# Optimization experiments

Hardware: AMD Instinct MI355X
Metric: run time of the kernel (lower is better)

Reference implementation:

```python
import jax, jax.numpy as jnp
import numpy as np

B, L, C = 8, 999, 768
C2 = C // 2           # 384 per branch
H, HD = 8, C2 // 8    # heads, head_dim=48
K, G = 3, 2           # dynamic conv kernel size, num_groups
DC_IN = C2 // 4       # DynamicConv1d proj inner (reduction_ratio default 4) = 96
PJ_IN = max(16, C // 8)  # mixer proj inner_dim = 96
SCALE = HD ** -0.5
EPS = 1e-5


def _gelu(x):
    return jax.nn.gelu(x, approximate=False)


def _c1x1(x, w, b):
    # pointwise conv1d: x (B,Cin,L), w (Cout,Cin), b (Cout,)
    return jnp.einsum('bcl,oc->bol', x, w) + b[None, :, None]


def _dw3(x, w, b):
    # depthwise conv1d k=3 pad=1: x (B,Ch,L), w (Ch,3), b (Ch,) or None
    Lx = x.shape[-1]
    xp = jnp.pad(x, ((0, 0), (0, 0), (1, 1)))
    y = (xp[:, :, 0:Lx] * w[:, 0][None, :, None]
         + xp[:, :, 1:Lx + 1] * w[:, 1][None, :, None]
         + xp[:, :, 2:Lx + 2] * w[:, 2][None, :, None])
    if b is not None:
        y = y + b[None, :, None]
    return y


def _bn(x, g, b):
    # BatchNorm1d, training-mode batch stats over (B, L): x (B,Ch,L)
    m = x.mean(axis=(0, 2), keepdims=True)
    v = ((x - m) ** 2).mean(axis=(0, 2), keepdims=True)
    return (x - m) * jax.lax.rsqrt(v + EPS) * g[None, :, None] + b[None, :, None]


def setup_inputs() -> dict:
    key = jax.random.key(0)
    ks = jax.random.split(key, 30)
    s = 0.02
    d = {
        'x': jax.random.normal(ks[0], (B, L, C), jnp.float32),
        # DynamicConv1d (dim=384, K=3, G=2, inner=96)
        'dc_weight': jax.random.normal(ks[1], (G, C2, K), jnp.float32) * s,
        'dc_bias':   jax.random.normal(ks[2], (G, C2), jnp.float32) * s,
        'dc_p1w':    jax.random.normal(ks[3], (DC_IN, C2), jnp.float32) * s,
        'dc_p1b':    jax.random.normal(ks[4], (DC_IN,), jnp.float32) * s,
        'dc_p2w':    jax.random.normal(ks[5], (C2 * G, DC_IN), jnp.float32) * s,
        'dc_p2b':    jax.random.normal(ks[6], (C2 * G,), jnp.float32) * s,
        # Attention (dim=384, heads=8, sr_ratio=1 -> sr=Identity)
        'at_qw':  jax.random.normal(ks[7], (C2, C2), jnp.float32) * s,
        'at_qb':  jax.random.normal(ks[8], (C2,), jnp.float32) * s,
        'at_kvw': jax.random.normal(ks[9], (2 * C2, C2), jnp.float32) * s,
        'at_kvb': jax.random.normal(ks[10], (2 * C2,), jnp.float32) * s,
        'at_lcw': jax.random.normal(ks[11], (C2, K), jnp.float32) * s,
        'at_lcb': jax.random.normal(ks[12], (C2,), jnp.float32) * s,
        # mixer proj
        'pj_dww':  jax.random.normal(ks[13], (C, K), jnp.float32) * s,
        'pj_dwb':  jax.random.normal(ks[14], (C,), jnp.float32) * s,
        'pj_bn1g': jnp.ones((C,), jnp.float32),
        'pj_bn1b': jnp.zeros((C,), jnp.float32),
        'pj_c1w':  jax.random.normal(ks[15], (PJ_IN, C), jnp.float32) * s,
        'pj_c1b':  jax.random.normal(ks[16], (PJ_IN,), jnp.float32) * s,
        'pj_bn2g': jnp.ones((PJ_IN,), jnp.float32),
        'pj_bn2b': jnp.zeros((PJ_IN,), jnp.float32),
        'pj_c2w':  jax.random.normal(ks[17], (C, PJ_IN), jnp.float32) * s,
        'pj_c2b':  jax.random.normal(ks[18], (C,), jnp.float32) * s,
        'pj_bn3g': jnp.ones((C,), jnp.float32),
        'pj_bn3b': jnp.zeros((C,), jnp.float32),
    }
    return d


def _dynamic_conv(x, dc_weight, dc_bias, p1w, p1b, p2w, p2b):
    # x: (B, L, C2)
    xt = jnp.transpose(x, (0, 2, 1))                 # (B,C2,L)
    # AdaptiveAvgPool1d(K) with L divisible by K -> exact non-overlapping mean
    pooled = xt.reshape(B, C2, K, L // K).mean(-1)   # (B,C2,K)
    sc = _c1x1(_gelu(_c1x1(pooled, p1w, p1b)), p2w, p2b)  # (B, G*C2, K)
    sc = jax.nn.softmax(sc.reshape(B, G, C2, K), axis=1)
    w = (sc * dc_weight[None]).sum(axis=1)           # (B,C2,K) per-sample kernels
    xm = xt.mean(axis=2, keepdims=True)              # (B,C2,1)
    sb = _c1x1(_gelu(_c1x1(xm, p1w, p1b)), p2w, p2b) # (B, G*C2, 1)
    sb = jax.nn.softmax(sb.reshape(B, G, C2), axis=1)
    bias = (sb * dc_bias[None]).sum(axis=1)          # (B,C2)
    # depthwise per-(b,c) conv, k=3, pad=1
    xp = jnp.pad(xt, ((0, 0), (0, 0), (1, 1)))
    y = (xp[:, :, 0:L] * w[:, :, 0:1]
         + xp[:, :, 1:L + 1] * w[:, :, 1:2]
         + xp[:, :, 2:L + 2] * w[:, :, 2:3]) + bias[:, :, None]
    return jnp.transpose(y, (0, 2, 1))               # (B,L,C2)


def _attention(x, qw, qb, kvw, kvb, lcw, lcb):
    # x: (B, L, C2)
    xt = jnp.transpose(x, (0, 2, 1))                 # (B,C2,L)
    q = _c1x1(xt, qw, qb).reshape(B, H, HD, L)
    q = jnp.transpose(q, (0, 1, 3, 2))               # (B,H,L,HD)
    kv_in = _dw3(xt, lcw, lcb) + xt                  # local_conv(kv)+kv (sr=Identity)
    kv = _c1x1(kv_in, kvw, kvb)                      # (B,2*C2,L)
    k = kv[:, :C2].reshape(B, H, HD, L)              # (B,H,HD,L)
    v = jnp.transpose(kv[:, C2:].reshape(B, H, HD, L), (0, 1, 3, 2))  # (B,H,L,HD)
    attn = jnp.einsum('bhld,bhdm->bhlm', q, k) * SCALE
    attn = jax.nn.softmax(attn, axis=-1)
    out = jnp.einsum('bhlm,bhmd->bhld', attn, v)     # (B,H,L,HD)
    # faithful to torch: transpose(-1,-2) then reshape(B, L, C2)
    out = jnp.transpose(out, (0, 1, 3, 2)).reshape(B, L, C2)
    return out


def reference(x, dc_weight, dc_bias, dc_p1w, dc_p1b, dc_p2w, dc_p2b,
              at_qw, at_qb, at_kvw, at_kvb, at_lcw, at_lcb,
              pj_dww, pj_dwb, pj_bn1g, pj_bn1b, pj_c1w, pj_c1b,
              pj_bn2g, pj_bn2b, pj_c2w, pj_c2b, pj_bn3g, pj_bn3b):
    x1 = x[:, :, :C2]
    x2 = x[:, :, C2:]
    x1 = _dynamic_conv(x1, dc_weight, dc_bias, dc_p1w, dc_p1b, dc_p2w, dc_p2b)
    x2 = _attention(x2, at_qw, at_qb, at_kvw, at_kvb, at_lcw, at_lcb)
    xc = jnp.concatenate([x1, x2], axis=2)           # (B,L,C)
    xt = jnp.transpose(xc, (0, 2, 1))                # (B,C,L)
    h = _bn(_gelu(_dw3(xt, pj_dww, pj_dwb)), pj_bn1g, pj_bn1b)
    h = _bn(_gelu(_c1x1(h, pj_c1w, pj_c1b)), pj_bn2g, pj_bn2b)
    h = _bn(_c1x1(h, pj_c2w, pj_c2b), pj_bn3g, pj_bn3b)
    out = h + xt
    return jnp.transpose(out, (0, 2, 1))             # (B,L,C)
```

## Files before the change

### kernel.cpp

```cpp
#include <hip/hip_runtime.h>
#include <cstddef>

constexpr int B = 8, L = 999, C = 768, C2 = 384, H = 8, HD = 48;
constexpr float ATT_SCALE = 0.14433756729740644f;
constexpr float LOG2E = 1.4426950408889634f;
constexpr float BN_EPS = 1e-5f;
constexpr float INV_N = 1.0f / (8.0f * 999.0f);

constexpr size_t SZ_XT   = (size_t)B * C * L;
constexpr size_t SZ_HALF = (size_t)B * C2 * L;
constexpr size_t OFF_XT  = 0;
constexpr size_t OFF_XT2 = SZ_XT;
constexpr size_t OFF_KV  = 2 * SZ_XT;
constexpr size_t OFF_AX  = 3 * SZ_XT;
constexpr size_t OFF_Q   = 3 * SZ_XT + SZ_HALF;
constexpr size_t OFF_SM  = 3 * SZ_XT + SZ_HALF + SZ_HALF / 2;

constexpr size_t SM_POOLED = 0;
constexpr size_t SM_XM     = 9216;
constexpr size_t SM_H1     = 12288;
constexpr size_t SM_WDYN   = 15360;
constexpr size_t SM_BDYN   = 24576;
constexpr size_t SM_SUM1   = 27648;
constexpr size_t SM_SQ1    = 28416;
constexpr size_t SM_S1     = 29184;
constexpr size_t SM_M1     = 29952;
constexpr size_t SM_CB1    = 30720;
constexpr size_t SM_SUM2   = 30816;
constexpr size_t SM_SQ2    = 30912;
constexpr size_t SM_S2     = 31008;
constexpr size_t SM_M2     = 31104;
constexpr size_t SM_CB2    = 31200;
constexpr size_t SM_SUM3   = 31968;
constexpr size_t SM_SQ3    = 32736;
constexpr size_t SM_S3     = 33504;
constexpr size_t SM_D3     = 34272;
constexpr size_t SM_END    = 35040;
constexpr size_t SM_WQ  = SM_END;
constexpr size_t SM_WKV = SM_WQ + 73728;
constexpr size_t SM_WC1 = SM_WKV + 147456;
constexpr size_t SM_WC2 = SM_WC1 + 36864;

typedef __attribute__((ext_vector_type(8))) short bf16x8;
typedef __attribute__((ext_vector_type(4))) float floatx4;

__device__ __forceinline__ float gelu_f(float x) {
  return 0.5f * x * (1.0f + erff(x * 0.70710678118654752f));
}

__device__ __forceinline__ float wave_sum(float v) {
  #pragma unroll
  for (int off = 32; off > 0; off >>= 1) v += __shfl_down(v, off, 64);
  return v;
}

__device__ __forceinline__ short f2bf(float f) {
  union { float f; unsigned u; } x; x.f = f;
  unsigned r = x.u + 0x7FFFu + ((x.u >> 16) & 1u);
  return (short)(r >> 16);
}

__device__ __forceinline__ bf16x8 pack8(const float* p) {
  union { unsigned u[4]; bf16x8 v; } r;
  asm("v_cvt_pk_bf16_f32 %0, %1, %2" : "=v"(r.u[0]) : "v"(p[0]), "v"(p[1]));
  asm("v_cvt_pk_bf16_f32 %0, %1, %2" : "=v"(r.u[1]) : "v"(p[2]), "v"(p[3]));
  asm("v_cvt_pk_bf16_f32 %0, %1, %2" : "=v"(r.u[2]) : "v"(p[4]), "v"(p[5]));
  asm("v_cvt_pk_bf16_f32 %0, %1, %2" : "=v"(r.u[3]) : "v"(p[6]), "v"(p[7]));
  return r.v;
}

__device__ __forceinline__ float exp2_hw(float x) {
  float r;
  asm("v_exp_f32 %0, %1" : "=v"(r) : "v"(x));
  return r;
}

__global__ void k_prep(const float* __restrict__ qw, short* __restrict__ wq,
                       const float* __restrict__ kvw, short* __restrict__ wkv,
                       const float* __restrict__ c1w, short* __restrict__ wc1,
                       const float* __restrict__ c2w, short* __restrict__ wc2,
                       const float* __restrict__ c1b, const float* __restrict__ bn1b,
                       const float* __restrict__ c2b, const float* __restrict__ bn2b,
                       float* __restrict__ cb1, float* __restrict__ cb2) {
  int bid = blockIdx.x;
  if (bid < 288) {
    const float* src; short* dst; int base;
    if (bid < 72)       { src = qw;  dst = wq;  base = bid; }
    else if (bid < 216) { src = kvw; dst = wkv; base = bid - 72; }
    else if (bid < 252) { src = c1w; dst = wc1; base = bid - 216; }
    else                { src = c2w; dst = wc2; base = bid - 252; }
    int i = (base * 256 + threadIdx.x) * 8;
    float4 a = *reinterpret_cast<const float4*>(&src[i]);
    float4 b = *reinterpret_cast<const float4*>(&src[i + 4]);
    short tmp[8] = {f2bf(a.x), f2bf(a.y), f2bf(a.z), f2bf(a.w),
                    f2bf(b.x), f2bf(b.y), f2bf(b.z), f2bf(b.w)};
    *(bf16x8*)&dst[i] = *(bf16x8*)tmp;
  } else if (bid == 288) {
    int o = threadIdx.x;
    if (o < 96) {
      float a = c1b[o];
      const float* wr = c1w + (size_t)o * C;
      for (int c = 0; c < C; c++) a += bn1b[c] * wr[c];
      cb1[o] = a;
    }
  } else {
    for (int o = threadIdx.x; o < C; o += 256) {
      float a = c2b[o];
      const float* wr = c2w + (size_t)o * 96;
      for (int i = 0; i < 96; i++) a += bn2b[i] * wr[i];
      cb2[o] = a;
    }
  }
}

__global__ __launch_bounds__(384) void k_kvin(const float* __restrict__ x,
                                              const float* __restrict__ lcw,
                                              const float* __restrict__ lcb,
                                              short* __restrict__ x2bf,
                                              short* __restrict__ kvinbf) {
  int b = blockIdx.y, l0 = blockIdx.x * 8, c = threadIdx.x;
  float w0 = lcw[c * 3], w1 = lcw[c * 3 + 1] + 1.0f, w2 = lcw[c * 3 + 2], bb = lcb[c];
  const float* xb = x + (size_t)b * L * C + C2 + c;
  float prev = (l0 > 0) ? xb[(size_t)(l0 - 1) * C] : 0.f;
  float cur  = (l0 < L) ? xb[(size_t)l0 * C] : 0.f;
  #pragma unroll
  for (int r = 0; r < 8; r++) {
    int l = l0 + r;
    if (l >= L) break;
    float nxt = (l + 1 < L) ? xb[(size_t)(l + 1) * C] : 0.f;
    x2bf[((size_t)b * L + l) * C2 + c]   = f2bf(cur);
    kvinbf[((size_t)b * L + l) * C2 + c] = f2bf(prev * w0 + cur * w1 + nxt * w2 + bb);
    prev = cur; cur = nxt;
  }
}

__global__ void k_transpose_in(const float* __restrict__ x, float* __restrict__ xt) {
  __shared__ float tile[32][33];
  int b = blockIdx.z;
  int l0 = blockIdx.x * 32, c0 = blockIdx.y * 32;
  int tx = threadIdx.x, ty = threadIdx.y;
  #pragma unroll
  for (int i = 0; i < 4; i++) {
    int l = l0 + ty + i * 8, c = c0 + tx;
    if (l < L) tile[ty + i * 8][tx] = x[((size_t)b * L + l) * C + c];
  }
  __syncthreads();
  #pragma unroll
  for (int i = 0; i < 4; i++) {
    int c = c0 + ty + i * 8, l = l0 + tx;
    if (l < L) xt[((size_t)b * C + c) * L + l] = tile[tx][ty + i * 8];
  }
}

__global__ __launch_bounds__(256) void k_pool(const float* __restrict__ xt,
                                              float* __restrict__ pooled,
                                              float* __restrict__ xm) {
  int c = blockIdx.x, b = blockIdx.y;
  const float* row = xt + ((size_t)b * C + c) * L;
  float s0 = 0.f, s1 = 0.f, s2 = 0.f;
  for (int l = threadIdx.x; l < L; l += 256) {
    float v = row[l];
    int ch = l / 333;
    if (ch == 0) s0 += v; else if (ch == 1) s1 += v; else s2 += v;
  }
  s0 = wave_sum(s0); s1 = wave_sum(s1); s2 = wave_sum(s2);
  __shared__ float r[3][4];
  int lane = threadIdx.x & 63, wid = threadIdx.x >> 6;
  if (lane == 0) { r[0][wid] = s0; r[1][wid] = s1; r[2][wid] = s2; }
  __syncthreads();
  if (threadIdx.x == 0) {
    float t0 = r[0][0] + r[0][1] + r[0][2] + r[0][3];
    float t1 = r[1][0] + r[1][1] + r[1][2] + r[1][3];
    float t2 = r[2][0] + r[2][1] + r[2][2] + r[2][3];
    size_t pb = (size_t)(b * C2 + c) * 3;
    pooled[pb + 0] = t0 / 333.f;
    pooled[pb + 1] = t1 / 333.f;
    pooled[pb + 2] = t2 / 333.f;
    xm[b * C2 + c] = (t0 + t1 + t2) / 999.f;
  }
}

__global__ void k_mlp1(const float* __restrict__ pooled, const float* __restrict__ xm,
                       const float* __restrict__ p1w, const float* __restrict__ p1b,
                       float* __restrict__ h1) {
  int j = blockIdx.x, b = blockIdx.y;
  __shared__ float vin[C2];
  for (int c = threadIdx.x; c < C2; c += 128)
    vin[c] = (j < 3) ? pooled[(size_t)(b * C2 + c) * 3 + j] : xm[b * C2 + c];
  __syncthreads();
  int o = threadIdx.x;
  if (o < 96) {
    float acc = p1b[o];
    const float* wr = p1w + (size_t)o * C2;
    for (int c = 0; c < C2; c++) acc += vin[c] * wr[c];
    h1[(b * 4 + j) * 96 + o] = gelu_f(acc);
  }
}

__global__ void k_mix2(const float* __restrict__ h1,
                       const float* __restrict__ p2w, const float* __restrict__ p2b,
                       const float* __restrict__ dcw, const float* __restrict__ dcb,
                       float* __restrict__ wdyn, float* __restrict__ bdyn) {
  int j = blockIdx.x, b = blockIdx.y;
  __shared__ float hv[96];
  for (int i = threadIdx.x; i < 96; i += 384) hv[i] = h1[(b * 4 + j) * 96 + i];
  __syncthreads();
  int c = threadIdx.x;
  float a0 = p2b[c], a1 = p2b[C2 + c];
  const float* w0r = p2w + (size_t)c * 96;
  const float* w1r = p2w + (size_t)(C2 + c) * 96;
  for (int i = 0; i < 96; i++) { float h = hv[i]; a0 += h * w0r[i]; a1 += h * w1r[i]; }
  float m = fmaxf(a0, a1);
  float e0 = __expf(a0 - m), e1 = __expf(a1 - m);
  float inv = 1.f / (e0 + e1);
  float p0 = e0 * inv, p1 = e1 * inv;
  if (j < 3)
    wdyn[(size_t)(b * C2 + c) * 3 + j] = p0 * dcw[(size_t)c * 3 + j] + p1 * dcw[(size_t)(C2 + c) * 3 + j];
  else
    bdyn[b * C2 + c] = p0 * dcb[c] + p1 * dcb[C2 + c];
}

__global__ __launch_bounds__(256) void k_dwconv(const float* __restrict__ xt,
                                                const float* __restrict__ wdyn,
                                                const float* __restrict__ bdyn,
                                                float* __restrict__ xt2) {
  int c = blockIdx.x, b = blockIdx.y;
  const float* rowA = xt + ((size_t)b * C + c) * L;
  size_t wb = (size_t)(b * C2 + c) * 3;
  float a0 = wdyn[wb], a1 = wdyn[wb + 1], a2 = wdyn[wb + 2], ab = bdyn[b * C2 + c];
  float* oA = xt2 + ((size_t)b * C + c) * L;
  for (int l = threadIdx.x; l < L; l += 256) {
    float xm1 = (l > 0) ? rowA[l - 1] : 0.f;
    float x0 = rowA[l];
    float xp1 = (l < L - 1) ? rowA[l + 1] : 0.f;
    oA[l] = xm1 * a0 + x0 * a1 + xp1 * a2 + ab;
  }
}

template<int LT, bool XBF16>
__global__ __launch_bounds__(256) void k_gemm3(const short* __restrict__ Wbf,
                                               const void* __restrict__ Xv,
                                               void* __restrict__ Yv,
                                               const float* __restrict__ shift,
                                               const float* __restrict__ scale,
                                               const float* __restrict__ bias,
                                               float* __restrict__ sum, float* __restrict__ sq,
                                               int O, int Kd, int Kstride, int XLd,
                                               size_t xbs, size_t ybs,
                                               int flags, float outmul,
                                               int ksplit, size_t slice) {
  __shared__ __align__(16) short Xt[2][LT * 72];
  constexpr int R = LT / 32;
  int b = blockIdx.z;
  int kc = (int)blockIdx.y % ksplit;
  int o0 = ((int)blockIdx.y / ksplit) * 64;
  int l0 = blockIdx.x * LT;
  int kbeg = kc * Kd;
  int t = threadIdx.x, w = t >> 6, lane = t & 63;
  int col = lane & 15, quad = lane >> 4;
  int KT = (Kd + 63) >> 6;

  floatx4 acc[LT / 16];
  #pragma unroll
  for (int i = 0; i < LT / 16; i++) acc[i] = floatx4{0.f, 0.f, 0.f, 0.f};

  int orow = o0 + w * 16 + col;
  bool wok = orow < O;
  const short* Wrow = Wbf + (size_t)orow * Kstride + kbeg;

  const short* Xb16 = (const short*)Xv + (size_t)b * xbs + kbeg;
  const float* Xb32 = (const float*)Xv + (size_t)b * xbs + kbeg;

  bf16x8 xr[R];
  float4 xf[R][2];
  bf16x8 wcur0, wcur1, wnxt0, wnxt1;

  auto xload = [&](int k0) {
    #pragma unroll
    for (int r = 0; r < R; r++) {
      int u = t + r * 256;
      int ll = u >> 3, oct = u & 7;
      int l = l0 + ll, kk = k0 + oct * 8;
      bool ok = (l < L) && (kk < Kd);
      if constexpr (XBF16) {
        xr[r] = ok ? *(const bf16x8*)&Xb16[(size_t)l * XLd + kk]
                   : bf16x8{0, 0, 0, 0, 0, 0, 0, 0};
      } else {
        if (ok) {
          const float* p = &Xb32[(size_t)l * XLd + kk];
          float4 a = *(const float4*)p;
          float4 bq = *(const float4*)(p + 4);
          if (shift) {
            float4 sh0 = *(const float4*)&shift[kbeg + kk];
            float4 sh1 = *(const float4*)&shift[kbeg + kk + 4];
            float4 sc0 = *(const float4*)&scale[kbeg + kk];
            float4 sc1 = *(const float4*)&scale[kbeg + kk + 4];
            a.x = (a.x - sh0.x) * sc0.x;  a.y = (a.y - sh0.y) * sc0.y;
            a.z = (a.z - sh0.z) * sc0.z;  a.w = (a.w - sh0.w) * sc0.w;
            bq.x = (bq.x - sh1.x) * sc1.x; bq.y = (bq.y - sh1.y) * sc1.y;
            bq.z = (bq.z - sh1.z) * sc1.z; bq.w = (bq.w - sh1.w) * sc1.w;
          }
          xf[r][0] = a;
          xf[r][1] = bq;
        } else {
          xf[r][0] = float4{0.f, 0.f, 0.f, 0.f};
          xf[r][1] = float4{0.f, 0.f, 0.f, 0.f};
        }
      }
    }
  };
  auto xwrite = [&](int buf) {
    #pragma unroll
    for (int r = 0; r < R; r++) {
      int u = t + r * 256;
      int ll = u >> 3, oct = u & 7;
      bf16x8 val;
      if constexpr (XBF16) {
        val = xr[r];
      } else {
        union { unsigned u4[4]; bf16x8 v; } pk;
        asm("v_cvt_pk_bf16_f32 %0, %1, %2" : "=v"(pk.u4[0]) : "v"(xf[r][0].x), "v"(xf[r][0].y));
        asm("v_cvt_pk_bf16_f32 %0, %1, %2" : "=v"(pk.u4[1]) : "v"(xf[r][0].z), "v"(xf[r][0].w));
        asm("v_cvt_pk_bf16_f32 %0, %1, %2" : "=v"(pk.u4[2]) : "v"(xf[r][1].x), "v"(xf[r][1].y));
        asm("v_cvt_pk_bf16_f32 %0, %1, %2" : "=v"(pk.u4[3]) : "v"(xf[r][1].z), "v"(xf[r][1].w));
        val = pk.v;
      }
      *(bf16x8*)&Xt[buf][ll * 72 + oct * 8] = val;
    }
  };
  auto wload = [&](int k0, bf16x8& f0, bf16x8& f1) {
    int kk0 = k0 + quad * 8;
    int kk1 = k0 + 32 + quad * 8;
    f0 = (wok && kk0 < Kd) ? *(const bf16x8*)&Wrow[kk0] : bf16x8{0, 0, 0, 0, 0, 0, 0, 0};
    f1 = (wok && kk1 < Kd) ? *(const bf16x8*)&Wrow[kk1] : bf16x8{0, 0, 0, 0, 0, 0, 0, 0};
  };

  xload(0);
  wload(0, wcur0, wcur1);
  xwrite(0);
  __syncthreads();

  for (int it = 0; it < KT; ++it) {
    int curb = it & 1;
    bool more = (it + 1 < KT);
    if (more) { xload((it + 1) * 64); wload((it + 1) * 64, wnxt0, wnxt1); }
    #pragma unroll
    for (int nt = 0; nt < LT / 16; nt++) {
      bf16x8 bx0 = *(bf16x8*)&Xt[curb][(nt * 16 + col) * 72 + quad * 8];
      acc[nt] = __builtin_amdgcn_mfma_f32_16x16x32_bf16(wcur0, bx0, acc[nt], 0, 0, 0);
      bf16x8 bx1 = *(bf16x8*)&Xt[curb][(nt * 16 + col) * 72 + 32 + quad * 8];
      acc[nt] = __builtin_amdgcn_mfma_f32_16x16x32_bf16(wcur1, bx1, acc[nt], 0, 0, 0);
    }
    if (more) xwrite(curb ^ 1);
    __syncthreads();
    wcur0 = wnxt0; wcur1 = wnxt1;
  }

  int o_base = o0 + w * 16 + quad * 4;
  #pragma unroll
  for (int r = 0; r < 4; r++) {
    int o = o_base + r;
    bool ov = o < O;
    float bo = (bias && ov) ? bias[o] : 0.f;
    float ps = 0.f, pq = 0.f;
    #pragma unroll
    for (int nt = 0; nt < LT / 16; nt++) {
      int l = l0 + nt * 16 + col;
      float v = acc[nt][r] + bo;
      if (flags & 1) v = gelu_f(v);
      v *= outmul;
      if (l >= L) v = 0.f;
      if (ov && l < L) {
        if (flags & 2) ((short*)Yv)[(size_t)b * ybs + (size_t)o * L + l] = f2bf(v);
        else           ((float*)Yv)[kc * slice + (size_t)b * ybs + (size_t)o * L + l] = v;
      }
      ps += v; pq += v * v;
    }
    if ((flags & 8) && ov) {
      ps += __shfl_xor(ps, 1); ps += __shfl_xor(ps, 2);
      ps += __shfl_xor(ps, 4); ps += __shfl_xor(ps, 8);
      pq += __shfl_xor(pq, 1); pq += __shfl_xor(pq, 2);
      pq += __shfl_xor(pq, 4); pq += __shfl_xor(pq, 8);
      if (col == 0) { atomicAdd(&sum[o], ps); atomicAdd(&sq[o], pq); }
    }
  }
}

__global__ __launch_bounds__(256) void k_h2fin_t(const float* __restrict__ part,
                                                 const float* __restrict__ cb1,
                                                 float* __restrict__ h2,
                                                 float* __restrict__ sum, float* __restrict__ sq) {
  __shared__ float tile[96][33];
  __shared__ float lsum[96], lsq[96];
  constexpr size_t SL = (size_t)B * 96 * L;
  int b = blockIdx.y, l0 = blockIdx.x * 32;
  int t = threadIdx.x;
  #pragma unroll
  for (int p = 0; p < 12; p++) {
    int u = t + p * 256;
    int o = u >> 5, li = u & 31;
    int l = l0 + li;
    float v = 0.f;
    if (l < L) {
      size_t idx = ((size_t)b * 96 + o) * L + l;
      v = gelu_f(part[idx] + part[SL + idx] + part[2 * SL + idx] + part[3 * SL + idx] + cb1[o]);
    }
    tile[o][li] = v;
    float vs = v, vq = v * v;
    vs += __shfl_xor(vs, 1); vs += __shfl_xor(vs, 2); vs += __shfl_xor(vs, 4);
    vs += __shfl_xor(vs, 8); vs += __shfl_xor(vs, 16);
    vq += __shfl_xor(vq, 1); vq += __shfl_xor(vq, 2); vq += __shfl_xor(vq, 4);
    vq += __shfl_xor(vq, 8); vq += __shfl_xor(vq, 16);
    if ((t & 31) == 0) { lsum[o] = vs; lsq[o] = vq; }
  }
  __syncthreads();
  if (t < 96) { atomicAdd(&sum[t], lsum[t]); atomicAdd(&sq[t], lsq[t]); }
  #pragma unroll
  for (int p = 0; p < 12; p++) {
    int u = t + p * 256;
    int lr = u / 96, o = u % 96;
    int l = l0 + lr;
    if (l < L) h2[((size_t)b * L + l) * 96 + o] = tile[o][lr];
  }
}

__global__ __launch_bounds__(512, 4) void k_attn_mfma(const short* __restrict__ q,
                                                      const short* __restrict__ kv,
                                                      float* __restrict__ out) {
  __shared__ __align__(16) char smem[2 * 8192 + 2 * 6144 + 33280];
  short* Ks0 = (short*)smem;
  short* Ks1 = (short*)(smem + 8192);
  short* Vf0 = (short*)(smem + 16384);
  short* Vf1 = (short*)(smem + 22528);
  float* PF  = (float*)(smem + 28672);
  float* Os  = (float*)smem;

  int lt0 = blockIdx.x * 128;
  int h = blockIdx.y, b = blockIdx.z;
  int t = threadIdx.x;
  int w = t >> 6, lane = t & 63;
  int col = lane & 15, quad = lane >> 4;
  const short* qb = q  + ((size_t)b * C2 + h * HD) * L;
  const short* kb = kv + ((size_t)b * C  + h * HD) * L;
  const short* vb = kv + ((size_t)b * C + C2 + h * HD) * L;

  bf16x8 aq0, aq1;
  {
    int l = lt0 + w * 16 + col;
    bool ok = l < L;
    const short* qp = qb + (size_t)(quad * 8) * L + l;
    short v0[8];
    #pragma unroll
    for (int jj = 0; jj < 8; jj++) v0[jj] = ok ? qp[(size_t)jj * L] : (short)0;
    aq0 = *(bf16x8*)v0;
    if (quad < 2) {
      const short* qp1 = qb + (size_t)(32 + quad * 8) * L + l;
      short v1[8];
      #pragma unroll
      for (int jj = 0; jj < 8; jj++) v1[jj] = ok ? qp1[(size_t)jj * L] : (short)0;
      aq1 = *(bf16x8*)v1;
    } else {
      aq1 = bf16x8{0, 0, 0, 0, 0, 0, 0, 0};
    }
  }

  short kreg[8];
  short vreg[8];

  auto stage_load = [&](int m0) {
    if (t < 384) {
      int m = t & 63, j = t >> 6;
      int gm = m0 + m;
      bool ok = gm < L;
      const short* src = kb + (size_t)(8 * j) * L + gm;
      #pragma unroll
      for (int jj = 0; jj < 8; jj++) kreg[jj] = ok ? src[(size_t)jj * L] : (short)0;
    }
    if (t >= 128) {
      int a = t - 128;
      int d = (a & 7) | ((a >> 6) << 3);
      int o = (a >> 3) & 7;
      int mb = m0 + o * 8;
      const short* src = vb + (size_t)d * L + mb;
      #pragma unroll
      for (int j = 0; j < 8; j++) vreg[j] = (mb + j < L) ? src[j] : (short)0;
    }
  };
  auto stage_write = [&](short* Kd, short* Vd) {
    if (t < 384) {
      int m = t & 63, j = t >> 6;
      int slot = ((m >> 4) * 2 + (j >> 2)) * 64 + (j & 3) * 16 + (m & 15);
      *(bf16x8*)&Kd[slot * 8] = *(bf16x8*)kreg;
    }
    if (t >= 128) {
      int a = t - 128;
      int d = (a & 7) | ((a >> 6) << 3);
      int o = (a >> 3) & 7;
      int lanep = ((o & 3) << 4) | (d & 15);
      *(bf16x8*)&Vd[(((o >> 2) * 3 + (d >> 4)) * 64 + lanep) * 8] = *(bf16x8*)vreg;
    }
  };

  if (t < 256) {
    int i = t & 127;
    int ms = i >> 5, qq = 2 + ((i >> 4) & 1), cc = i & 15;
    int slot = (ms * 2 + 1) * 64 + qq * 16 + cc;
    short* Kd = (t < 128) ? Ks0 : Ks1;
    *(bf16x8*)&Kd[slot * 8] = bf16x8{0, 0, 0, 0, 0, 0, 0, 0};
  }

  stage_load(0);
  stage_write(Ks0, Vf0);

  floatx4 of[3];
  #pragma unroll
  for (int i = 0; i < 3; i++) of[i] = floatx4{0.f, 0.f, 0.f, 0.f};
  float rs[4] = {0.f, 0.f, 0.f, 0.f};
  __syncthreads();

  for (int it = 0; it < 16; ++it) {
    int m0 = it * 64;
    short* Kc = (it & 1) ? Ks1 : Ks0;
    short* Vc = (it & 1) ? Vf1 : Vf0;
    short* Kn = (it & 1) ? Ks0 : Ks1;
    short* Vn = (it & 1) ? Vf0 : Vf1;
    if (it < 15) stage_load(m0 + 64);

    floatx4 sf[4];
    __builtin_amdgcn_s_setprio(1);
    #pragma unroll
    for (int ms = 0; ms < 4; ms++) {
      bf16x8 bk0 = *(bf16x8*)&Kc[((ms * 2 + 0) * 64 + lane) * 8];
      bf16x8 bk1 = *(bf16x8*)&Kc[((ms * 2 + 1) * 64 + lane) * 8];
      floatx4 a4 = floatx4{0.f, 0.f, 0.f, 0.f};
      a4 = __builtin_amdgcn_mfma_f32_16x16x32_bf16(aq0, bk0, a4, 0, 0, 0);
      a4 = __builtin_amdgcn_mfma_f32_16x16x32_bf16(aq1, bk1, a4, 0, 0, 0);
      sf[ms] = a4;
    }
    __builtin_amdgcn_s_setprio(0);

    float* pw = PF + w * 1040 + lane;
    #pragma unroll
    for (int ms = 0; ms < 4; ms++) {
      int m = m0 + ms * 16 + col;
      bool ok = m < L;
      #pragma unroll
      for (int r = 0; r < 4; r++) {
        float e = ok ? exp2_hw(sf[ms][r]) : 0.f;
        rs[r] += e;
        pw[(ms * 4 + r) * 65] = e;
      }
    }

    const float* pr = PF + w * 1040 + (col & 3) * 65 + (col >> 2) * 16 + (quad & 1) * 8;
    __builtin_amdgcn_s_setprio(1);
    #pragma unroll
    for (int mh = 0; mh < 2; mh++) {
      const float* ps = pr + (mh * 2 + (quad >> 1)) * 260;
      float p8[8];
      #pragma unroll
      for (int jj = 0; jj < 8; jj++) p8[jj] = ps[jj];
      bf16x8 ap = pack8(p8);
      #pragma unroll
      for (int ds = 0; ds < 3; ds++) {
        bf16x8 bv = *(bf16x8*)&Vc[((mh * 3 + ds) * 64 + lane) * 8];
        of[ds] = __builtin_amdgcn_mfma_f32_16x16x32_bf16(ap, bv, of[ds], 0, 0, 0);
      }
    }
    __builtin_amdgcn_s_setprio(0);
    if (it < 15) stage_write(Kn, Vn);
    __syncthreads();
  }

  #pragma unroll
  for (int r = 0; r < 4; r++) {
    float v = rs[r];
    v += __shfl_xor(v, 1); v += __shfl_xor(v, 2);
    v += __shfl_xor(v, 4); v += __shfl_xor(v, 8);
    rs[r] = v;
  }
  #pragma unroll
  for (int r = 0; r < 4; r++) {
    float inv = 1.f / rs[r];
    #pragma unroll
    for (int ds = 0; ds < 3; ds++)
      Os[(ds * 16 + col) * 130 + w * 16 + quad * 4 + r] = of[ds][r] * inv;
  }
  __syncthreads();
  for (int i = t; i < 48 * 128; i += 512) {
    int d = i >> 7, ll = i & 127;
    int l = lt0 + ll;
    if (l < L) out[((size_t)b * C2 + h * HD + d) * L + l] = Os[d * 130 + ll];
  }
}

__global__ void k_fill_xt2(const float* __restrict__ ao, float* __restrict__ xt2) {
  __shared__ float tile[32][33];
  int b = blockIdx.z;
  int l0 = blockIdx.x * 32, c0 = blockIdx.y * 32;
  int tx = threadIdx.x, ty = threadIdx.y;
  #pragma unroll
  for (int i = 0; i < 4; i++) {
    int l = l0 + ty + i * 8, c = c0 + tx;
    if (l < L) tile[ty + i * 8][tx] = ao[(size_t)b * ((size_t)L * C2) + (size_t)l * C2 + c];
  }
  __syncthreads();
  #pragma unroll
  for (int i = 0; i < 4; i++) {
    int c = c0 + ty + i * 8, l = l0 + tx;
    if (l < L) xt2[((size_t)b * C + C2 + c) * L + l] = tile[tx][ty + i * 8];
  }
}

__global__ __launch_bounds__(256) void k_dwproj_t(const float* __restrict__ xt2,
                                                  const float* __restrict__ dww,
                                                  const float* __restrict__ dwb,
                                                  float* __restrict__ t1,
                                                  float* __restrict__ sum, float* __restrict__ sq) {
  __shared__ float tile[32][67];
  __shared__ float rs[4][32], rq[4][32];
  int b = blockIdx.z, c0 = blockIdx.y * 32, l0 = blockIdx.x * 64;
  int t = threadIdx.x;
  for (int u = t; u < 32 * 66; u += 256) {
    int cc = u / 66, li = u % 66;
    int l = l0 - 1 + li;
    tile[cc][li] = (l >= 0 && l < L) ? xt2[((size_t)b * C + c0 + cc) * L + l] : 0.f;
  }
  __syncthreads();
  int c = c0 + (t & 31);
  float w0 = dww[c * 3], w1 = dww[c * 3 + 1], w2 = dww[c * 3 + 2], bb = dwb[c];
  int cc = t & 31;
  float s = 0.f, s2 = 0.f;
  #pragma unroll
  for (int p = 0; p < 8; p++) {
    int lr = (t >> 5) + p * 8;
    int l = l0 + lr;
    float v = 0.f;
    if (l < L) {
      v = gelu_f(tile[cc][lr] * w0 + tile[cc][lr + 1] * w1 + tile[cc][lr + 2] * w2 + bb);
      t1[((size_t)b * L + l) * C + c] = v;
    }
    s += v; s2 += v * v;
  }
  s += __shfl_xor(s, 32, 64); s2 += __shfl_xor(s2, 32, 64);
  int wv = t >> 6, ln = t & 63;
  if (ln < 32) { rs[wv][ln] = s; rq[wv][ln] = s2; }
  __syncthreads();
  if (t < 32) {
    float a = rs[0][t] + rs[1][t] + rs[2][t] + rs[3][t];
    float qq = rq[0][t] + rq[1][t] + rq[2][t] + rq[3][t];
    atomicAdd(&sum[c0 + t], a);
    atomicAdd(&sq[c0 + t], qq);
  }
}

__global__ void k_bnfin(const float* __restrict__ sum, const float* __restrict__ sq,
                        const float* __restrict__ g, int n,
                        float* __restrict__ s_, float* __restrict__ m_) {
  int t = threadIdx.x;
  if (t < n) {
    float m = sum[t] * INV_N;
    float v = sq[t] * INV_N - m * m;
    float r = rsqrtf(v + BN_EPS);
    s_[t] = g[t] * r;
    m_[t] = m;
  }
}

__global__ void k_fin3(const float* __restrict__ sum, const float* __restrict__ sq,
                       const float* __restrict__ g, const float* __restrict__ be,
                       float* __restrict__ s3, float* __restrict__ d3) {
  int t = threadIdx.x;
  if (t < C) {
    float m = sum[t] * INV_N;
    float v = sq[t] * INV_N - m * m;
    float r = rsqrtf(v + BN_EPS);
    float sc = g[t] * r;
    s3[t] = sc;
    d3[t] = be[t] - m * sc;
  }
}

__global__ void k_final(const float* __restrict__ y3, const float* __restrict__ xt2,
                        const float* __restrict__ s3, const float* __restrict__ d3,
                        float* __restrict__ out) {
  __shared__ float tile[32][33];
  int b = blockIdx.z;
  int l0 = blockIdx.x * 32, c0 = blockIdx.y * 32;
  int tx = threadIdx.x, ty = threadIdx.y;
  #pragma unroll
  for (int i = 0; i < 4; i++) {
    int c = c0 + ty + i * 8, l = l0 + tx;
    if (l < L) {
      size_t idx = ((size_t)b * C + c) * L + l;
      tile[ty + i * 8][tx] = y3[idx] * s3[c] + d3[c] + xt2[idx];
    }
  }
  __syncthreads();
  #pragma unroll
  for (int i = 0; i < 4; i++) {
    int l = l0 + ty + i * 8, c = c0 + tx;
    if (l < L) out[((size_t)b * L + l) * C + c] = tile[tx][ty + i * 8];
  }
}

extern "C" void kernel_launch(void* const* d_in, const int* in_sizes, int n_in,
                              void* d_out, int out_size, void* d_ws, size_t ws_size,
                              hipStream_t stream) {
  const float* x    = (const float*)d_in[0];
  const float* dcw  = (const float*)d_in[1];
  const float* dcb  = (const float*)d_in[2];
  const float* p1w  = (const float*)d_in[3];
  const float* p1b  = (const float*)d_in[4];
  const float* p2w  = (const float*)d_in[5];
  const float* p2b  = (const float*)d_in[6];
  const float* qw   = (const float*)d_in[7];
  const float* qb   = (const float*)d_in[8];
  const float* kvw  = (const float*)d_in[9];
  const float* kvb  = (const float*)d_in[10];
  const float* lcw  = (const float*)d_in[11];
  const float* lcb  = (const float*)d_in[12];
  const float* dww  = (const float*)d_in[13];
  const float* dwb  = (const float*)d_in[14];
  const float* bn1g = (const float*)d_in[15];
  const float* bn1b = (const float*)d_in[16];
  const float* c1w  = (const float*)d_in[17];
  const float* c1b  = (const float*)d_in[18];
  const float* bn2g = (const float*)d_in[19];
  const float* bn2b = (const float*)d_in[20];
  const float* c2w  = (const float*)d_in[21];
  const float* c2b  = (const float*)d_in[22];
  const float* bn3g = (const float*)d_in[23];
  const float* bn3b = (const float*)d_in[24];
  float* out = (float*)d_out;
  float* ws  = (float*)d_ws;

  float* xt      = ws + OFF_XT;
  float* xt2     = ws + OFF_XT2;
  short* kvbuf   = (short*)(ws + OFF_KV);
  float* y3      = ws + OFF_KV;
  short* x2bf    = (short*)(ws + OFF_AX);
  short* kvinbf  = (short*)(ws + OFF_AX + SZ_HALF / 2);
  float* attnout = ws + OFF_AX;
  float* c1part  = ws + OFF_AX;
  short* qbuf    = (short*)(ws + OFF_Q);
  float* h2      = ws + OFF_Q;
  float* sm      = ws + OFF_SM;

  float* pooled = sm + SM_POOLED;
  float* xm     = sm + SM_XM;
  float* h1     = sm + SM_H1;
  float* wdyn   = sm + SM_WDYN;
  float* bdyn   = sm + SM_BDYN;
  float* sum1 = sm + SM_SUM1; float* sq1 = sm + SM_SQ1;
  float* s1 = sm + SM_S1; float* m1 = sm + SM_M1; float* cb1 = sm + SM_CB1;
  float* sum2 = sm + SM_SUM2; float* sq2 = sm + SM_SQ2;
  float* s2 = sm + SM_S2; float* m2 = sm + SM_M2; float* cb2 = sm + SM_CB2;
  float* sum3 = sm + SM_SUM3; float* sq3 = sm + SM_SQ3;
  float* s3 = sm + SM_S3; float* d3 = sm + SM_D3;
  short* wqbf  = (short*)(sm + SM_WQ);
  short* wkvbf = (short*)(sm + SM_WKV);
  short* wc1bf = (short*)(sm + SM_WC1);
  short* wc2bf = (short*)(sm + SM_WC2);

  hipMemsetAsync((void*)(sm + SM_SUM1), 0, (SM_S3 - SM_SUM1) * sizeof(float), stream);

  k_prep<<<290, 256, 0, stream>>>(qw, wqbf, kvw, wkvbf, c1w, wc1bf, c2w, wc2bf,
                                  c1b, bn1b, c2b, bn2b, cb1, cb2);
  k_kvin<<<dim3(125, B), 384, 0, stream>>>(x, lcw, lcb, x2bf, kvinbf);

  dim3 tb32(32, 8);
  k_transpose_in<<<dim3(32, 12, B), tb32, 0, stream>>>(x, xt);
  k_pool<<<dim3(C2, B), 256, 0, stream>>>(xt, pooled, xm);
  k_mlp1<<<dim3(4, B), 128, 0, stream>>>(pooled, xm, p1w, p1b, h1);
  k_mix2<<<dim3(4, B), 384, 0, stream>>>(h1, p2w, p2b, dcw, dcb, wdyn, bdyn);
  k_dwconv<<<dim3(C2, B), 256, 0, stream>>>(xt, wdyn, bdyn, xt2);
  k_gemm3<64, true><<<dim3(16, 6, B), 256, 0, stream>>>(
      wqbf, (const void*)x2bf, (void*)qbuf, nullptr, nullptr, qb, nullptr, nullptr,
      C2, C2, C2, C2, (size_t)C2 * L, (size_t)C2 * L, 2, ATT_SCALE * LOG2E, 1, 0);
  k_gemm3<128, true><<<dim3(8, 12, B), 256, 0, stream>>>(
      wkvbf, (const void*)kvinbf, (void*)kvbuf, nullptr, nullptr, kvb, nullptr, nullptr,
      C, C2, C2, C2, (size_t)C2 * L, (size_t)C * L, 2, 1.0f, 1, 0);
  k_attn_mfma<<<dim3(8, H, B), 512, 0, stream>>>(qbuf, kvbuf, attnout);
  k_fill_xt2<<<dim3(32, 12, B), tb32, 0, stream>>>(attnout, xt2);
  k_dwproj_t<<<dim3(16, 24, B), 256, 0, stream>>>(xt2, dww, dwb, xt, sum1, sq1);
  k_bnfin<<<1, 768, 0, stream>>>(sum1, sq1, bn1g, C, s1, m1);
  k_gemm3<128, false><<<dim3(8, 8, B), 256, 0, stream>>>(
      wc1bf, (const void*)xt, (void*)c1part, m1, s1, nullptr, nullptr, nullptr,
      96, 192, C, C, (size_t)C * L, (size_t)96 * L, 0, 1.0f, 4, (size_t)B * 96 * L);
  k_h2fin_t<<<dim3(32, B), 256, 0, stream>>>(c1part, cb1, h2, sum2, sq2);
  k_bnfin<<<1, 768, 0, stream>>>(sum2, sq2, bn2g, 96, s2, m2);
  k_gemm3<128, false><<<dim3(8, 12, B), 256, 0, stream>>>(
      wc2bf, (const void*)h2, (void*)y3, m2, s2, cb2, sum3, sq3,
      C, 96, 96, 96, (size_t)96 * L, (size_t)C * L, 8, 1.0f, 1, 0);
  k_fin3<<<1, 768, 0, stream>>>(sum3, sq3, bn3g, bn3b, s3, d3);
  k_final<<<dim3(32, 24, B), tb32, 0, stream>>>(y3, xt2, s3, d3, out);
}
```

Measured before the change: 353.7 us.

## Widen GEMM output tiles and pad KV rows for vectorized V loads

k_gemm3 gains an OT template parameter so each block computes 128 output rows. This reuses each shared-memory X tile across two weight slices and halves the grid for the Q, KV and conv2 GEMMs. The KV projection now writes rows with a padded stride of 1000, so the attention kernel can load V with aligned 16-byte vector loads instead of 8 scalar shorts. The fp32-to-bf16 conversion moves from the LDS write step into the global load step. Costs are more accumulator registers, which can lower occupancy, and fewer blocks in flight.

```diff
diff --git a/kernel.cpp b/kernel.cpp
--- a/kernel.cpp
+++ b/kernel.cpp
@@ -2,6 +2,7 @@
 #include <cstddef>
 
 constexpr int B = 8, L = 999, C = 768, C2 = 384, H = 8, HD = 48;
+constexpr int KVL = 1000;
 constexpr float ATT_SCALE = 0.14433756729740644f;
 constexpr float LOG2E = 1.4426950408889634f;
 constexpr float BN_EPS = 1e-5f;
@@ -237,7 +238,7 @@
   }
 }
 
-template<int LT, bool XBF16>
+template<int LT, int OT, bool XBF16>
 __global__ __launch_bounds__(256) void k_gemm3(const short* __restrict__ Wbf,
                                                const void* __restrict__ Xv,
                                                void* __restrict__ Yv,
@@ -245,35 +246,42 @@
                                                const float* __restrict__ scale,
                                                const float* __restrict__ bias,
                                                float* __restrict__ sum, float* __restrict__ sq,
-                                               int O, int Kd, int Kstride, int XLd,
+                                               int O, int Kd, int Kstride, int XLd, int Ldy,
                                                size_t xbs, size_t ybs,
                                                int flags, float outmul,
                                                int ksplit, size_t slice) {
   __shared__ __align__(16) short Xt[2][LT * 72];
   constexpr int R = LT / 32;
+  constexpr int NS = OT / 64;
   int b = blockIdx.z;
   int kc = (int)blockIdx.y % ksplit;
-  int o0 = ((int)blockIdx.y / ksplit) * 64;
+  int o0 = ((int)blockIdx.y / ksplit) * OT;
   int l0 = blockIdx.x * LT;
   int kbeg = kc * Kd;
   int t = threadIdx.x, w = t >> 6, lane = t & 63;
   int col = lane & 15, quad = lane >> 4;
   int KT = (Kd + 63) >> 6;
 
-  floatx4 acc[LT / 16];
-  #pragma unroll
-  for (int i = 0; i < LT / 16; i++) acc[i] = floatx4{0.f, 0.f, 0.f, 0.f};
-
-  int orow = o0 + w * 16 + col;
-  bool wok = orow < O;
-  const short* Wrow = Wbf + (size_t)orow * Kstride + kbeg;
+  floatx4 acc[NS][LT / 16];
+  #pragma unroll
+  for (int s = 0; s < NS; s++)
+    #pragma unroll
+    for (int i = 0; i < LT / 16; i++) acc[s][i] = floatx4{0.f, 0.f, 0.f, 0.f};
+
+  bool wok[NS];
+  const short* Wrow[NS];
+  #pragma unroll
+  for (int s = 0; s < NS; s++) {
+    int orow = o0 + s * 64 + w * 16 + col;
+    wok[s] = orow < O;
+    Wrow[s] = Wbf + (size_t)orow * Kstride + kbeg;
+  }
 
   const short* Xb16 = (const short*)Xv + (size_t)b * xbs + kbeg;
   const float* Xb32 = (const float*)Xv + (size_t)b * xbs + kbeg;
 
   bf16x8 xr[R];
-  float4 xf[R][2];
-  bf16x8 wcur0, wcur1, wnxt0, wnxt1;
+  bf16x8 wcur[NS][2], wnxt[NS][2];
 
   auto xload = [&](int k0) {
     #pragma unroll
@@ -300,11 +308,14 @@
             bq.x = (bq.x - sh1.x) * sc1.x; bq.y = (bq.y - sh1.y) * sc1.y;
             bq.z = (bq.z - sh1.z) * sc1.z; bq.w = (bq.w - sh1.w) * sc1.w;
           }
-          xf[r][0] = a;
-          xf[r][1] = bq;
+          union { unsigned u4[4]; bf16x8 v; } pk;
+          asm("v_cvt_pk_bf16_f32 %0, %1, %2" : "=v"(pk.u4[0]) : "v"(a.x), "v"(a.y));
+          asm("v_cvt_pk_bf16_f32 %0, %1, %2" : "=v"(pk.u4[1]) : "v"(a.z), "v"(a.w));
+          asm("v_cvt_pk_bf16_f32 %0, %1, %2" : "=v"(pk.u4[2]) : "v"(bq.x), "v"(bq.y));
+          asm("v_cvt_pk_bf16_f32 %0, %1, %2" : "=v"(pk.u4[3]) : "v"(bq.z), "v"(bq.w));
+          xr[r] = pk.v;
         } else {
-          xf[r][0] = float4{0.f, 0.f, 0.f, 0.f};
-          xf[r][1] = float4{0.f, 0.f, 0.f, 0.f};
+          xr[r] = bf16x8{0, 0, 0, 0, 0, 0, 0, 0};
         }
       }
     }
@@ -314,74 +325,74 @@
     for (int r = 0; r < R; r++) {
       int u = t + r * 256;
       int ll = u >> 3, oct = u & 7;
-      bf16x8 val;
-      if constexpr (XBF16) {
-        val = xr[r];
-      } else {
-        union { unsigned u4[4]; bf16x8 v; } pk;
-        asm("v_cvt_pk_bf16_f32 %0, %1, %2" : "=v"(pk.u4[0]) : "v"(xf[r][0].x), "v"(xf[r][0].y));
-        asm("v_cvt_pk_bf16_f32 %0, %1, %2" : "=v"(pk.u4[1]) : "v"(xf[r][0].z), "v"(xf[r][0].w));
-        asm("v_cvt_pk_bf16_f32 %0, %1, %2" : "=v"(pk.u4[2]) : "v"(xf[r][1].x), "v"(xf[r][1].y));
-        asm("v_cvt_pk_bf16_f32 %0, %1, %2" : "=v"(pk.u4[3]) : "v"(xf[r][1].z), "v"(xf[r][1].w));
-        val = pk.v;
-      }
-      *(bf16x8*)&Xt[buf][ll * 72 + oct * 8] = val;
+      *(bf16x8*)&Xt[buf][ll * 72 + oct * 8] = xr[r];
     }
   };
-  auto wload = [&](int k0, bf16x8& f0, bf16x8& f1) {
+  auto wload = [&](int k0, bf16x8 (&f)[NS][2]) {
     int kk0 = k0 + quad * 8;
     int kk1 = k0 + 32 + quad * 8;
-    f0 = (wok && kk0 < Kd) ? *(const bf16x8*)&Wrow[kk0] : bf16x8{0, 0, 0, 0, 0, 0, 0, 0};
-    f1 = (wok && kk1 < Kd) ? *(const bf16x8*)&Wrow[kk1] : bf16x8{0, 0, 0, 0, 0, 0, 0, 0};
+    #pragma unroll
+    for (int s = 0; s < NS; s++) {
+      f[s][0] = (wok[s] && kk0 < Kd) ? *(const bf16x8*)&Wrow[s][kk0] : bf16x8{0, 0, 0, 0, 0, 0, 0, 0};
+      f[s][1] = (wok[s] && kk1 < Kd) ? *(const bf16x8*)&Wrow[s][kk1] : bf16x8{0, 0, 0, 0, 0, 0, 0, 0};
+    }
   };
 
   xload(0);
-  wload(0, wcur0, wcur1);
+  wload(0, wcur);
   xwrite(0);
   __syncthreads();
 
   for (int it = 0; it < KT; ++it) {
     int curb = it & 1;
     bool more = (it + 1 < KT);
-    if (more) { xload((it + 1) * 64); wload((it + 1) * 64, wnxt0, wnxt1); }
+    if (more) { xload((it + 1) * 64); wload((it + 1) * 64, wnxt); }
     #pragma unroll
     for (int nt = 0; nt < LT / 16; nt++) {
       bf16x8 bx0 = *(bf16x8*)&Xt[curb][(nt * 16 + col) * 72 + quad * 8];
-      acc[nt] = __builtin_amdgcn_mfma_f32_16x16x32_bf16(wcur0, bx0, acc[nt], 0, 0, 0);
+      #pragma unroll
+      for (int s = 0; s < NS; s++)
+        acc[s][nt] = __builtin_amdgcn_mfma_f32_16x16x32_bf16(wcur[s][0], bx0, acc[s][nt], 0, 0, 0);
       bf16x8 bx1 = *(bf16x8*)&Xt[curb][(nt * 16 + col) * 72 + 32 + quad * 8];
-      acc[nt] = __builtin_amdgcn_mfma_f32_16x16x32_bf16(wcur1, bx1, acc[nt], 0, 0, 0);
+      #pragma unroll
+      for (int s = 0; s < NS; s++)
+        acc[s][nt] = __builtin_amdgcn_mfma_f32_16x16x32_bf16(wcur[s][1], bx1, acc[s][nt], 0, 0, 0);
     }
     if (more) xwrite(curb ^ 1);
     __syncthreads();
-    wcur0 = wnxt0; wcur1 = wnxt1;
-  }
-
-  int o_base = o0 + w * 16 + quad * 4;
-  #pragma unroll
-  for (int r = 0; r < 4; r++) {
-    int o = o_base + r;
-    bool ov = o < O;
-    float bo = (bias && ov) ? bias[o] : 0.f;
-    float ps = 0.f, pq = 0.f;
-    #pragma unroll
-    for (int nt = 0; nt < LT / 16; nt++) {
-      int l = l0 + nt * 16 + col;
-      float v = acc[nt][r] + bo;
-      if (flags & 1) v = gelu_f(v);
-      v *= outmul;
-      if (l >= L) v = 0.f;
-      if (ov && l < L) {
-        if (flags & 2) ((short*)Yv)[(size_t)b * ybs + (size_t)o * L + l] = f2bf(v);
-        else           ((float*)Yv)[kc * slice + (size_t)b * ybs + (size_t)o * L + l] = v;
+    #pragma unroll
+    for (int s = 0; s < NS; s++) { wcur[s][0] = wnxt[s][0]; wcur[s][1] = wnxt[s][1]; }
+  }
+
+  #pragma unroll
+  for (int s = 0; s < NS; s++) {
+    int o_base = o0 + s * 64 + w * 16 + quad * 4;
+    #pragma unroll
+    for (int r = 0; r < 4; r++) {
+      int o = o_base + r;
+      bool ov = o < O;
+      float bo = (bias && ov) ? bias[o] : 0.f;
+      float ps = 0.f, pq = 0.f;
+      #pragma unroll
+      for (int nt = 0; nt < LT / 16; nt++) {
+        int l = l0 + nt * 16 + col;
+        float v = acc[s][nt][r] + bo;
+        if (flags & 1) v = gelu_f(v);
+        v *= outmul;
+        if (l >= L) v = 0.f;
+        if (ov && l < L) {
+          if (flags & 2) ((short*)Yv)[(size_t)b * ybs + (size_t)o * Ldy + l] = f2bf(v);
+          else           ((float*)Yv)[kc * slice + (size_t)b * ybs + (size_t)o * Ldy + l] = v;
+        }
+        ps += v; pq += v * v;
       }
-      ps += v; pq += v * v;
-    }
-    if ((flags & 8) && ov) {
-      ps += __shfl_xor(ps, 1); ps += __shfl_xor(ps, 2);
-      ps += __shfl_xor(ps, 4); ps += __shfl_xor(ps, 8);
-      pq += __shfl_xor(pq, 1); pq += __shfl_xor(pq, 2);
-      pq += __shfl_xor(pq, 4); pq += __shfl_xor(pq, 8);
-      if (col == 0) { atomicAdd(&sum[o], ps); atomicAdd(&sq[o], pq); }
+      if ((flags & 8) && ov) {
+        ps += __shfl_xor(ps, 1); ps += __shfl_xor(ps, 2);
+        ps += __shfl_xor(ps, 4); ps += __shfl_xor(ps, 8);
+        pq += __shfl_xor(pq, 1); pq += __shfl_xor(pq, 2);
+        pq += __shfl_xor(pq, 4); pq += __shfl_xor(pq, 8);
+        if (col == 0) { atomicAdd(&sum[o], ps); atomicAdd(&sq[o], pq); }
+      }
     }
   }
 }
@@ -441,8 +452,8 @@
   int w = t >> 6, lane = t & 63;
   int col = lane & 15, quad = lane >> 4;
   const short* qb = q  + ((size_t)b * C2 + h * HD) * L;
-  const short* kb = kv + ((size_t)b * C  + h * HD) * L;
-  const short* vb = kv + ((size_t)b * C + C2 + h * HD) * L;
+  const short* kb = kv + ((size_t)b * C  + h * HD) * KVL;
+  const short* vb = kv + ((size_t)b * C + C2 + h * HD) * KVL;
 
   bf16x8 aq0, aq1;
   {
@@ -465,25 +476,31 @@
   }
 
   short kreg[8];
-  short vreg[8];
+  bf16x8 vreg;
 
   auto stage_load = [&](int m0) {
     if (t < 384) {
       int m = t & 63, j = t >> 6;
       int gm = m0 + m;
       bool ok = gm < L;
-      const short* src = kb + (size_t)(8 * j) * L + gm;
+      const short* src = kb + (size_t)(8 * j) * KVL + gm;
       #pragma unroll
-      for (int jj = 0; jj < 8; jj++) kreg[jj] = ok ? src[(size_t)jj * L] : (short)0;
+      for (int jj = 0; jj < 8; jj++) kreg[jj] = ok ? src[(size_t)jj * KVL] : (short)0;
     }
     if (t >= 128) {
       int a = t - 128;
       int d = (a & 7) | ((a >> 6) << 3);
       int o = (a >> 3) & 7;
       int mb = m0 + o * 8;
-      const short* src = vb + (size_t)d * L + mb;
-      #pragma unroll
-      for (int j = 0; j < 8; j++) vreg[j] = (mb + j < L) ? src[j] : (short)0;
+      const short* src = vb + (size_t)d * KVL + mb;
+      if (mb + 8 <= L) {
+        vreg = *(const bf16x8*)src;
+      } else {
+        short tmp[8];
+        #pragma unroll
+        for (int j = 0; j < 8; j++) tmp[j] = (mb + j < L) ? src[j] : (short)0;
+        vreg = *(bf16x8*)tmp;
+      }
     }
   };
   auto stage_write = [&](short* Kd, short* Vd) {
@@ -497,7 +514,7 @@
       int d = (a & 7) | ((a >> 6) << 3);
       int o = (a >> 3) & 7;
       int lanep = ((o & 3) << 4) | (d & 15);
-      *(bf16x8*)&Vd[(((o >> 2) * 3 + (d >> 4)) * 64 + lanep) * 8] = *(bf16x8*)vreg;
+      *(bf16x8*)&Vd[(((o >> 2) * 3 + (d >> 4)) * 64 + lanep) * 8] = vreg;
     }
   };
 
@@ -775,24 +792,24 @@
   k_mlp1<<<dim3(4, B), 128, 0, stream>>>(pooled, xm, p1w, p1b, h1);
   k_mix2<<<dim3(4, B), 384, 0, stream>>>(h1, p2w, p2b, dcw, dcb, wdyn, bdyn);
   k_dwconv<<<dim3(C2, B), 256, 0, stream>>>(xt, wdyn, bdyn, xt2);
-  k_gemm3<64, true><<<dim3(16, 6, B), 256, 0, stream>>>(
+  k_gemm3<64, 128, true><<<dim3(16, 3, B), 256, 0, stream>>>(
       wqbf, (const void*)x2bf, (void*)qbuf, nullptr, nullptr, qb, nullptr, nullptr,
-      C2, C2, C2, C2, (size_t)C2 * L, (size_t)C2 * L, 2, ATT_SCALE * LOG2E, 1, 0);
-  k_gemm3<128, true><<<dim3(8, 12, B), 256, 0, stream>>>(
+      C2, C2, C2, C2, L, (size_t)C2 * L, (size_t)C2 * L, 2, ATT_SCALE * LOG2E, 1, 0);
+  k_gemm3<128, 128, true><<<dim3(8, 6, B), 256, 0, stream>>>(
       wkvbf, (const void*)kvinbf, (void*)kvbuf, nullptr, nullptr, kvb, nullptr, nullptr,
-      C, C2, C2, C2, (size_t)C2 * L, (size_t)C * L, 2, 1.0f, 1, 0);
+      C, C2, C2, C2, KVL, (size_t)C2 * L, (size_t)C * KVL, 2, 1.0f, 1, 0);
   k_attn_mfma<<<dim3(8, H, B), 512, 0, stream>>>(qbuf, kvbuf, attnout);
   k_fill_xt2<<<dim3(32, 12, B), tb32, 0, stream>>>(attnout, xt2);
   k_dwproj_t<<<dim3(16, 24, B), 256, 0, stream>>>(xt2, dww, dwb, xt, sum1, sq1);
   k_bnfin<<<1, 768, 0, stream>>>(sum1, sq1, bn1g, C, s1, m1);
-  k_gemm3<128, false><<<dim3(8, 8, B), 256, 0, stream>>>(
+  k_gemm3<128, 64, false><<<dim3(8, 8, B), 256, 0, stream>>>(
       wc1bf, (const void*)xt, (void*)c1part, m1, s1, nullptr, nullptr, nullptr,
-      96, 192, C, C, (size_t)C * L, (size_t)96 * L, 0, 1.0f, 4, (size_t)B * 96 * L);
+      96, 192, C, C, L, (size_t)C * L, (size_t)96 * L, 0, 1.0f, 4, (size_t)B * 96 * L);
   k_h2fin_t<<<dim3(32, B), 256, 0, stream>>>(c1part, cb1, h2, sum2, sq2);
   k_bnfin<<<1, 768, 0, stream>>>(sum2, sq2, bn2g, 96, s2, m2);
-  k_gemm3<128, false><<<dim3(8, 12, B), 256, 0, stream>>>(
+  k_gemm3<128, 128, false><<<dim3(8, 6, B), 256, 0, stream>>>(
       wc2bf, (const void*)h2, (void*)y3, m2, s2, cb2, sum3, sq3,
-      C, 96, 96, 96, (size_t)96 * L, (size_t)C * L, 8, 1.0f, 1, 0);
+      C, 96, 96, 96, L, (size_t)96 * L, (size_t)C * L, 8, 1.0f, 1, 0);
   k_fin3<<<1, 768, 0, stream>>>(sum3, sq3, bn3g, bn3b, s3, d3);
   k_final<<<dim3(32, 24, B), tb32, 0, stream>>>(y3, xt2, s3, d3, out);
 }
```

After: 498.0 us. 1.41x slower.
